# Optimization experiments

Measured on AMD Instinct MI355X. Metric: run time of the kernel, lower is better.

Reference implementation:

```python
import jax, jax.numpy as jnp
import numpy as np
from jax import lax

B, T, K = 1024, 512, 32


def setup_inputs() -> dict:
    key = jax.random.key(0)
    k1, k2, k3 = jax.random.split(key, 3)
    labels = jax.random.randint(k1, (B, T), 0, K, dtype=jnp.int32)
    y_pred = jax.random.normal(k2, (B, T, K), dtype=jnp.float32)
    # glorot-uniform-ish transition matrix
    limit = np.sqrt(6.0 / (K + K)).astype(np.float32)
    trans = jax.random.uniform(k3, (K, K), minval=-limit, maxval=limit, dtype=jnp.float32)
    mask = jnp.ones((B, T), dtype=jnp.float32)
    return {"labels": labels, "y_pred": y_pred, "trans": trans, "mask": mask}


def crf_loss(labels, y_pred, trans, mask):
    n_tags = trans.shape[0]
    y_true = jax.nn.one_hot(labels, n_tags, dtype=y_pred.dtype)  # [B,T,K]
    y_true = y_true * mask[:, :, None]  # sequence_masking with value 0

    # --- target path score ---
    point_score = jnp.einsum('bni,bni->b', y_true, y_pred)
    trans_score = jnp.einsum('bni,ij,bnj->b', y_true[:, :-1], trans, y_true[:, 1:])
    target = point_score + trans_score

    # --- log partition via forward algorithm (logsumexp scan) ---
    alpha0 = y_pred[:, 0]  # [B,K]

    def step(alpha, xs):
        emit, m = xs  # emit: [B,K], m: [B,1]
        new = jax.nn.logsumexp(alpha[:, :, None] + trans[None], axis=1) + emit
        alpha = m * new + (1.0 - m) * alpha
        return alpha, None

    xs = (jnp.swapaxes(y_pred[:, 1:], 0, 1),          # [T-1,B,K]
          jnp.swapaxes(mask[:, 1:, None], 0, 1))      # [T-1,B,1]
    alpha, _ = lax.scan(step, alpha0, xs)
    log_norm = jax.nn.logsumexp(alpha, axis=1)  # [B]
    return log_norm - target


def reference(labels, y_pred, trans, mask):
    return crf_loss(labels, y_pred, trans, mask)
```

## Files before the change

kernel.cpp:

```cpp
#include <hip/hip_runtime.h>


#define K32 32
#define Tt  512
#define NCH 4
#define CHL 128
#define NSEG 2

typedef float  float4v __attribute__((ext_vector_type(4)));
typedef short  short8v __attribute__((ext_vector_type(8)));

__device__ inline float bf2f_lo(unsigned d) { return __uint_as_float(d << 16); }
__device__ inline float bf2f_hi(unsigned d) { return __uint_as_float(d & 0xFFFF0000u); }

__device__ inline unsigned pack_trunc(float hi, float lo) {
    return __builtin_amdgcn_perm(__float_as_uint(hi), __float_as_uint(lo), 0x07060302u);
}
__device__ inline unsigned short f2bf_rne(float x) {
    unsigned u = __float_as_uint(x);
    return (unsigned short)((u + 0x7FFFu + ((u >> 16) & 1u)) >> 16);
}

union F8 { unsigned u[4]; short8v v; };

__global__ __launch_bounds__(256, 4) void crf_fused(
    const int*   __restrict__ labels,
    const float* __restrict__ y_pred,
    const float* __restrict__ trans,
    const float* __restrict__ mask,
    float*       __restrict__ out)
{
    __shared__ float expAll[4][2048];

    const int lane = threadIdx.x & 63;
    const int wv   = __builtin_amdgcn_readfirstlane(threadIdx.x >> 6);
    const int n    = lane & 15;
    const int q    = lane >> 4;
    const int seq  = blockIdx.x;
    const int c    = wv;

    float* eb = &expAll[wv][0];

    const float* yp  = y_pred + (size_t)seq * Tt * K32;
    const int*   lb  = labels + (size_t)seq * Tt;
    const float* mkp = mask   + (size_t)seq * Tt;
    const int tbase = c * CHL;

    float4 pre[8];
    {
        const float4* gs = (const float4*)(yp + (size_t)tbase * K32);
#pragma unroll
        for (int jj = 0; jj < 8; ++jj) pre[jj] = gs[jj * 64 + lane];
    }

    unsigned long long mb[NSEG];
    float sc = 0.0f;
#pragma unroll
    for (int s = 0; s < NSEG; ++s) {
        const int t = tbase + s * 64 + lane;
        const int lab0 = lb[t];
        const float mlane = mkp[t];
        float scl = yp[t * K32 + lab0] * mlane;
        if (t < Tt - 1) {
            scl += trans[lab0 * K32 + lb[t + 1]] * (mlane * mkp[t + 1]);
        }
        sc += scl;
        mb[s] = __ballot(mlane != 0.0f);
    }
    if (c == 0) mb[0] &= ~1ull;
#pragma unroll
    for (int s = 1; s < 64; s <<= 1) sc += __shfl_xor(sc, s, 64);

    F8 AE0, AE1;
#pragma unroll
    for (int h = 0; h < 4; ++h) {
        const int k0 = (h < 2) ? (q * 4 + 2 * h) : (16 + q * 4 + 2 * (h - 2));
        const int k1 = k0 + 1;
        AE0.u[h] = ((unsigned)f2bf_rne(__expf(trans[k0 * K32 + n]) * 0.03125f)) |
                   (((unsigned)f2bf_rne(__expf(trans[k1 * K32 + n]) * 0.03125f)) << 16);
        AE1.u[h] = ((unsigned)f2bf_rne(__expf(trans[k0 * K32 + 16 + n]) * 0.03125f)) |
                   (((unsigned)f2bf_rne(__expf(trans[k1 * K32 + 16 + n]) * 0.03125f)) << 16);
    }

    F8 B0, B1;
#pragma unroll
    for (int h = 0; h < 4; ++h) {
        const int r0 = (h < 2) ? (q * 4 + 2 * h) : (16 + q * 4 + 2 * (h - 2));
        const int r1 = r0 + 1;
        unsigned w0 = 0, w1 = 0;
        if (r0 == n)      w0 |= 0x3F80u;
        if (r1 == n)      w0 |= 0x3F800000u;
        if (r0 == 16 + n) w1 |= 0x3F80u;
        if (r1 == 16 + n) w1 |= 0x3F800000u;
        B0.u[h] = w0;
        B1.u[h] = w1;
    }

    float Slog    = 0.0f;
    int   applied = 0;

    const int svoff0 = q * 4;
    const int svoff1 = 16 + q * 4;

    auto body = [&](int i) {
        const float4v sv0 = *(const float4v*)&eb[i * 32 + svoff0];
        const float4v sv1 = *(const float4v*)&eb[i * 32 + svoff1];

        float4v c00 = {0.f, 0.f, 0.f, 0.f}, c01 = {0.f, 0.f, 0.f, 0.f};
        float4v c10 = {0.f, 0.f, 0.f, 0.f}, c11 = {0.f, 0.f, 0.f, 0.f};
        c00 = __builtin_amdgcn_mfma_f32_16x16x32_bf16(AE0.v, B0.v, c00, 0, 0, 0);
        c01 = __builtin_amdgcn_mfma_f32_16x16x32_bf16(AE0.v, B1.v, c01, 0, 0, 0);
        c10 = __builtin_amdgcn_mfma_f32_16x16x32_bf16(AE1.v, B0.v, c10, 0, 0, 0);
        c11 = __builtin_amdgcn_mfma_f32_16x16x32_bf16(AE1.v, B1.v, c11, 0, 0, 0);

        c00 *= sv0; c01 *= sv0; c10 *= sv1; c11 *= sv1;

        if ((applied & 7) == 7) {
            const float cn = __uint_as_float(
                __builtin_amdgcn_readfirstlane(__float_as_uint(c00[0])));
            const float rs = 1.0f / cn;
            c00 *= rs; c01 *= rs; c10 *= rs; c11 *= rs;
            Slog += __logf(cn);
        }
        ++applied;

        B0.u[0] = pack_trunc(c00[1], c00[0]);
        B0.u[1] = pack_trunc(c00[3], c00[2]);
        B0.u[2] = pack_trunc(c10[1], c10[0]);
        B0.u[3] = pack_trunc(c10[3], c10[2]);
        B1.u[0] = pack_trunc(c01[1], c01[0]);
        B1.u[1] = pack_trunc(c01[3], c01[2]);
        B1.u[2] = pack_trunc(c11[1], c11[0]);
        B1.u[3] = pack_trunc(c11[3], c11[2]);
    };

    for (int seg = 0; seg < NSEG; ++seg) {
#pragma unroll
        for (int jj = 0; jj < 8; ++jj) {
            float4v e;
            e[0] = __expf(pre[jj].x); e[1] = __expf(pre[jj].y);
            e[2] = __expf(pre[jj].z); e[3] = __expf(pre[jj].w);
            *(float4v*)&eb[(jj * 64 + lane) * 4] = e;
        }
        if (seg + 1 < NSEG) {
            const float4* gs = (const float4*)(yp + (size_t)(tbase + (seg + 1) * 64) * K32);
#pragma unroll
            for (int jj = 0; jj < 8; ++jj) pre[jj] = gs[jj * 64 + lane];
        }

        const unsigned long long mbits = mb[seg];
        if (mbits == ~0ull) {
#pragma unroll 8
            for (int i = 0; i < 64; ++i) body(i);
        } else {
#pragma unroll 4
            for (int i = 0; i < 64; ++i) {
                if ((mbits >> i) & 1ull) body(i);
            }
        }
    }

    {
        unsigned* Nd = (unsigned*)eb + 1024;
        *(uint2*)&Nd[n * 20 + q * 2]            = make_uint2(B0.u[0], B0.u[1]);
        *(uint2*)&Nd[n * 20 + 8 + q * 2]        = make_uint2(B0.u[2], B0.u[3]);
        *(uint2*)&Nd[(16 + n) * 20 + q * 2]     = make_uint2(B1.u[0], B1.u[1]);
        *(uint2*)&Nd[(16 + n) * 20 + 8 + q * 2] = make_uint2(B1.u[2], B1.u[3]);
    }
    {
        const unsigned short* Ncm = (const unsigned short*)((unsigned*)eb + 1024);
        unsigned* md = (unsigned*)eb;
        for (int idx = lane; idx < 512; idx += 64) {
            const int k = idx >> 4, d = idx & 15;
            const unsigned lo = Ncm[(2 * d) * 40 + k];
            const unsigned hi = Ncm[(2 * d + 1) * 40 + k];
            md[idx] = lo | (hi << 16);
        }
    }
    if (lane == 0) {
        eb[1984] = Slog + (float)applied * 3.46573590f;
        eb[1985] = sc;
    }

    __syncthreads();

    if (wv == 0) {
        const int h = lane >> 5;
        const int j = lane & 31;

        uint4 mA[NCH], mB[NCH];
#pragma unroll
        for (int cc = 0; cc < NCH; ++cc) {
            const unsigned* mt = (const unsigned*)&expAll[cc][0];
            mA[cc] = *(const uint4*)&mt[j * 16 + 8 * h];
            mB[cc] = *(const uint4*)&mt[j * 16 + 8 * h + 4];
        }

        const float a0 = yp[j];
        const float m0 = __shfl(a0, 0, 64);
        float p = __expf(a0 - m0);
        float S = m0;

        float scs = 0.0f;
#pragma unroll
        for (int cc = 0; cc < NCH; ++cc) {
            S   += expAll[cc][1984];
            scs += expAll[cc][1985];
        }

        const int cb = h << 4;
#pragma unroll
        for (int cc = 0; cc < NCH; ++cc) {
            const float cn = __shfl(p, 0, 64);
            const unsigned u0 = mA[cc].x, u1 = mA[cc].y, u2 = mA[cc].z, u3 = mA[cc].w;
            const unsigned u4 = mB[cc].x, u5 = mB[cc].y, u6 = mB[cc].z, u7 = mB[cc].w;
            float acc = 0.0f;
            acc = fmaf(__shfl(p, cb +  0, 64), bf2f_lo(u0), acc);
            acc = fmaf(__shfl(p, cb +  1, 64), bf2f_hi(u0), acc);
            acc = fmaf(__shfl(p, cb +  2, 64), bf2f_lo(u1), acc);
            acc = fmaf(__shfl(p, cb +  3, 64), bf2f_hi(u1), acc);
            acc = fmaf(__shfl(p, cb +  4, 64), bf2f_lo(u2), acc);
            acc = fmaf(__shfl(p, cb +  5, 64), bf2f_hi(u2), acc);
            acc = fmaf(__shfl(p, cb +  6, 64), bf2f_lo(u3), acc);
            acc = fmaf(__shfl(p, cb +  7, 64), bf2f_hi(u3), acc);
            acc = fmaf(__shfl(p, cb +  8, 64), bf2f_lo(u4), acc);
            acc = fmaf(__shfl(p, cb +  9, 64), bf2f_hi(u4), acc);
            acc = fmaf(__shfl(p, cb + 10, 64), bf2f_lo(u5), acc);
            acc = fmaf(__shfl(p, cb + 11, 64), bf2f_hi(u5), acc);
            acc = fmaf(__shfl(p, cb + 12, 64), bf2f_lo(u6), acc);
            acc = fmaf(__shfl(p, cb + 13, 64), bf2f_hi(u6), acc);
            acc = fmaf(__shfl(p, cb + 14, 64), bf2f_lo(u7), acc);
            acc = fmaf(__shfl(p, cb + 15, 64), bf2f_hi(u7), acc);
            acc += __shfl_xor(acc, 32, 64);
            p = acc * (1.0f / cn);
            S += __logf(cn);
        }

        float sp = p;
        sp += __shfl_xor(sp,  1, 64);
        sp += __shfl_xor(sp,  2, 64);
        sp += __shfl_xor(sp,  4, 64);
        sp += __shfl_xor(sp,  8, 64);
        sp += __shfl_xor(sp, 16, 64);

        if (lane == 0) {
            out[seq] = S + __logf(sp) - scs;
        }
    }
}

extern "C" void kernel_launch(void* const* d_in, const int* in_sizes, int n_in,
                              void* d_out, int out_size, void* d_ws, size_t ws_size,
                              hipStream_t stream) {
    const int*   labels = (const int*)  d_in[0];
    const float* y_pred = (const float*)d_in[1];
    const float* trans  = (const float*)d_in[2];
    const float* mask   = (const float*)d_in[3];
    float* out = (float*)d_out;

    crf_fused<<<1024, 256, 0, stream>>>(labels, y_pred, trans, mask, out);
}
```

Baseline: 141.5 us.

## Split each sequence into eight 64-step chunks across eight wavefronts

Each block now handles one sequence with 8 wavefronts, each running a 64-timestep chunk of the forward recurrence, where before 4 wavefronts each ran 128 steps. This halves the serial matrix-product chain per wave and uses 32-step staging of exp(emissions) without register prefetch. The cost is a longer final combine of 8 chunk matrices in wave 0, with the next matrix now loaded one step ahead inside that loop. It also raises block size and launch bounds, which adds register pressure.

After: 141.2 us. About the same (-0.2%).

```diff
diff --git a/kernel.cpp b/kernel.cpp
--- a/kernel.cpp
+++ b/kernel.cpp
@@ -3,9 +3,10 @@
 
 #define K32 32
 #define Tt  512
-#define NCH 4
-#define CHL 128
-#define NSEG 2
+#define NCH 8
+#define CHL 64
+#define NST 2
+#define STL 32
 
 typedef float  float4v __attribute__((ext_vector_type(4)));
 typedef short  short8v __attribute__((ext_vector_type(8)));
@@ -23,14 +24,14 @@
 
 union F8 { unsigned u[4]; short8v v; };
 
-__global__ __launch_bounds__(256, 4) void crf_fused(
+__global__ __launch_bounds__(512, 8) void crf_fused(
     const int*   __restrict__ labels,
     const float* __restrict__ y_pred,
     const float* __restrict__ trans,
     const float* __restrict__ mask,
     float*       __restrict__ out)
 {
-    __shared__ float expAll[4][2048];
+    __shared__ float expAll[8][1024];
 
     const int lane = threadIdx.x & 63;
     const int wv   = __builtin_amdgcn_readfirstlane(threadIdx.x >> 6);
@@ -46,30 +47,21 @@
     const float* mkp = mask   + (size_t)seq * Tt;
     const int tbase = c * CHL;
 
-    float4 pre[8];
+    float sc;
+    float mlane;
     {
-        const float4* gs = (const float4*)(yp + (size_t)tbase * K32);
-#pragma unroll
-        for (int jj = 0; jj < 8; ++jj) pre[jj] = gs[jj * 64 + lane];
-    }
-
-    unsigned long long mb[NSEG];
-    float sc = 0.0f;
-#pragma unroll
-    for (int s = 0; s < NSEG; ++s) {
-        const int t = tbase + s * 64 + lane;
+        const int t = tbase + lane;
         const int lab0 = lb[t];
-        const float mlane = mkp[t];
-        float scl = yp[t * K32 + lab0] * mlane;
+        mlane = mkp[t];
+        sc = yp[t * K32 + lab0] * mlane;
         if (t < Tt - 1) {
-            scl += trans[lab0 * K32 + lb[t + 1]] * (mlane * mkp[t + 1]);
-        }
-        sc += scl;
-        mb[s] = __ballot(mlane != 0.0f);
-    }
-    if (c == 0) mb[0] &= ~1ull;
-#pragma unroll
-    for (int s = 1; s < 64; s <<= 1) sc += __shfl_xor(sc, s, 64);
+            sc += trans[lab0 * K32 + lb[t + 1]] * (mlane * mkp[t + 1]);
+        }
+#pragma unroll
+        for (int s = 1; s < 64; s <<= 1) sc += __shfl_xor(sc, s, 64);
+    }
+    unsigned long long mbits = __ballot(mlane != 0.0f);
+    if (c == 0) mbits &= ~1ull;
 
     F8 AE0, AE1;
 #pragma unroll
@@ -134,52 +126,53 @@
         B1.u[3] = pack_trunc(c11[3], c11[2]);
     };
 
-    for (int seg = 0; seg < NSEG; ++seg) {
-#pragma unroll
-        for (int jj = 0; jj < 8; ++jj) {
+    for (int st = 0; st < NST; ++st) {
+        const float4* gs = (const float4*)(yp + (size_t)(tbase + st * STL) * K32);
+#pragma unroll
+        for (int jj = 0; jj < 4; ++jj) {
+            const float4 pv = gs[jj * 64 + lane];
             float4v e;
-            e[0] = __expf(pre[jj].x); e[1] = __expf(pre[jj].y);
-            e[2] = __expf(pre[jj].z); e[3] = __expf(pre[jj].w);
+            e[0] = __expf(pv.x); e[1] = __expf(pv.y);
+            e[2] = __expf(pv.z); e[3] = __expf(pv.w);
             *(float4v*)&eb[(jj * 64 + lane) * 4] = e;
         }
-        if (seg + 1 < NSEG) {
-            const float4* gs = (const float4*)(yp + (size_t)(tbase + (seg + 1) * 64) * K32);
-#pragma unroll
-            for (int jj = 0; jj < 8; ++jj) pre[jj] = gs[jj * 64 + lane];
-        }
-
-        const unsigned long long mbits = mb[seg];
-        if (mbits == ~0ull) {
+
+        const unsigned b32 = (unsigned)(mbits >> (st * 32));
+        if (b32 == 0xFFFFFFFFu) {
 #pragma unroll 8
-            for (int i = 0; i < 64; ++i) body(i);
+            for (int i = 0; i < STL; ++i) body(i);
         } else {
 #pragma unroll 4
-            for (int i = 0; i < 64; ++i) {
-                if ((mbits >> i) & 1ull) body(i);
+            for (int i = 0; i < STL; ++i) {
+                if ((b32 >> i) & 1u) body(i);
             }
         }
     }
 
     {
-        unsigned* Nd = (unsigned*)eb + 1024;
+        unsigned* Nd = (unsigned*)eb;
         *(uint2*)&Nd[n * 20 + q * 2]            = make_uint2(B0.u[0], B0.u[1]);
         *(uint2*)&Nd[n * 20 + 8 + q * 2]        = make_uint2(B0.u[2], B0.u[3]);
         *(uint2*)&Nd[(16 + n) * 20 + q * 2]     = make_uint2(B1.u[0], B1.u[1]);
         *(uint2*)&Nd[(16 + n) * 20 + 8 + q * 2] = make_uint2(B1.u[2], B1.u[3]);
     }
     {
-        const unsigned short* Ncm = (const unsigned short*)((unsigned*)eb + 1024);
+        const unsigned short* Ncm = (const unsigned short*)eb;
+        unsigned r[8];
+#pragma unroll
+        for (int ii = 0; ii < 8; ++ii) {
+            const int idx = ii * 64 + lane;
+            const int k = idx >> 4, d = idx & 15;
+            r[ii] = (unsigned)Ncm[(2 * d) * 40 + k] |
+                    ((unsigned)Ncm[(2 * d + 1) * 40 + k] << 16);
+        }
         unsigned* md = (unsigned*)eb;
-        for (int idx = lane; idx < 512; idx += 64) {
-            const int k = idx >> 4, d = idx & 15;
-            const unsigned lo = Ncm[(2 * d) * 40 + k];
-            const unsigned hi = Ncm[(2 * d + 1) * 40 + k];
-            md[idx] = lo | (hi << 16);
-        }
+#pragma unroll
+        for (int ii = 0; ii < 8; ++ii) md[ii * 64 + lane] = r[ii];
     }
     if (lane == 0) {
-        eb[1984] = Slog + (float)applied * 3.46573590f;
-        eb[1985] = sc;
+        eb[1016] = Slog + (float)applied * 3.46573590f;
+        eb[1017] = sc;
     }
 
     __syncthreads();
@@ -188,12 +181,11 @@
         const int h = lane >> 5;
         const int j = lane & 31;
 
-        uint4 mA[NCH], mB[NCH];
-#pragma unroll
-        for (int cc = 0; cc < NCH; ++cc) {
-            const unsigned* mt = (const unsigned*)&expAll[cc][0];
-            mA[cc] = *(const uint4*)&mt[j * 16 + 8 * h];
-            mB[cc] = *(const uint4*)&mt[j * 16 + 8 * h + 4];
+        uint4 cA, cB;
+        {
+            const unsigned* mt = (const unsigned*)&expAll[0][0];
+            cA = *(const uint4*)&mt[j * 16 + 8 * h];
+            cB = *(const uint4*)&mt[j * 16 + 8 * h + 4];
         }
 
         const float a0 = yp[j];
@@ -204,16 +196,22 @@
         float scs = 0.0f;
 #pragma unroll
         for (int cc = 0; cc < NCH; ++cc) {
-            S   += expAll[cc][1984];
-            scs += expAll[cc][1985];
+            S   += expAll[cc][1016];
+            scs += expAll[cc][1017];
         }
 
         const int cb = h << 4;
 #pragma unroll
         for (int cc = 0; cc < NCH; ++cc) {
+            uint4 nA = {0, 0, 0, 0}, nB = {0, 0, 0, 0};
+            if (cc + 1 < NCH) {
+                const unsigned* mt = (const unsigned*)&expAll[cc + 1][0];
+                nA = *(const uint4*)&mt[j * 16 + 8 * h];
+                nB = *(const uint4*)&mt[j * 16 + 8 * h + 4];
+            }
             const float cn = __shfl(p, 0, 64);
-            const unsigned u0 = mA[cc].x, u1 = mA[cc].y, u2 = mA[cc].z, u3 = mA[cc].w;
-            const unsigned u4 = mB[cc].x, u5 = mB[cc].y, u6 = mB[cc].z, u7 = mB[cc].w;
+            const unsigned u0 = cA.x, u1 = cA.y, u2 = cA.z, u3 = cA.w;
+            const unsigned u4 = cB.x, u5 = cB.y, u6 = cB.z, u7 = cB.w;
             float acc = 0.0f;
             acc = fmaf(__shfl(p, cb +  0, 64), bf2f_lo(u0), acc);
             acc = fmaf(__shfl(p, cb +  1, 64), bf2f_hi(u0), acc);
@@ -234,6 +232,7 @@
             acc += __shfl_xor(acc, 32, 64);
             p = acc * (1.0f / cn);
             S += __logf(cn);
+            cA = nA; cB = nB;
         }
 
         float sp = p;
@@ -258,5 +257,5 @@
     const float* mask   = (const float*)d_in[3];
     float* out = (float*)d_out;
 
-    crf_fused<<<1024, 256, 0, stream>>>(labels, y_pred, trans, mask, out);
-}
+    crf_fused<<<1024, 512, 0, stream>>>(labels, y_pred, trans, mask, out);
+}
```

## Batch 16 sequences per wave in serial MFMA scan, split score kernel

Applied to the files above, without the earlier changes.

Replaces the chunked per-sequence matrix-product scan with one wave per group of 16 sequences. The wave performs a serial matrix-vector forward recursion using MFMA, with double-buffered global loads and exponent-based renormalisation. The target path score moves into a separate kernel that writes to workspace. This removes the chunk-combine phase and the shared-memory staging, but it launches only 64 single-wave blocks and runs a 511-step serial dependency chain, which risks low occupancy and exposed memory latency.

Result: slower. 171.8 us (+21.4%).

```diff
diff --git a/kernel.cpp b/kernel.cpp
--- a/kernel.cpp
+++ b/kernel.cpp
@@ -3,9 +3,7 @@
 
 #define K32 32
 #define Tt  512
-#define NCH 4
-#define CHL 128
-#define NSEG 2
+#define SB  16
 
 typedef float  float4v __attribute__((ext_vector_type(4)));
 typedef short  short8v __attribute__((ext_vector_type(8)));
@@ -23,229 +21,199 @@
 
 union F8 { unsigned u[4]; short8v v; };
 
-__global__ __launch_bounds__(256, 4) void crf_fused(
+__global__ __launch_bounds__(64) void crf_score(
     const int*   __restrict__ labels,
     const float* __restrict__ y_pred,
     const float* __restrict__ trans,
     const float* __restrict__ mask,
+    float*       __restrict__ wsScore)
+{
+    const int s    = blockIdx.x;
+    const int lane = threadIdx.x;
+    const int*   lb  = labels + (size_t)s * Tt;
+    const float* mkp = mask   + (size_t)s * Tt;
+    const float* yp  = y_pred + (size_t)s * Tt * K32;
+
+    float sc = 0.0f;
+#pragma unroll
+    for (int j = 0; j < 8; ++j) {
+        const int t   = j * 64 + lane;
+        const int lab = lb[t];
+        const float m = mkp[t];
+        sc += yp[t * K32 + lab] * m;
+        if (t < Tt - 1) sc += trans[lab * K32 + lb[t + 1]] * (m * mkp[t + 1]);
+    }
+#pragma unroll
+    for (int sft = 1; sft < 64; sft <<= 1) sc += __shfl_xor(sc, sft, 64);
+    if (lane == 0) wsScore[s] = sc;
+}
+
+__global__ __launch_bounds__(64) void crf_scan(
+    const float* __restrict__ y_pred,
+    const float* __restrict__ trans,
+    const float* __restrict__ mask,
+    const float* __restrict__ wsScore,
     float*       __restrict__ out)
 {
-    __shared__ float expAll[4][2048];
-
-    const int lane = threadIdx.x & 63;
-    const int wv   = __builtin_amdgcn_readfirstlane(threadIdx.x >> 6);
+    const int lane = threadIdx.x;
     const int n    = lane & 15;
-    const int q    = lane >> 4;
-    const int seq  = blockIdx.x;
-    const int c    = wv;
-
-    float* eb = &expAll[wv][0];
-
-    const float* yp  = y_pred + (size_t)seq * Tt * K32;
-    const int*   lb  = labels + (size_t)seq * Tt;
-    const float* mkp = mask   + (size_t)seq * Tt;
-    const int tbase = c * CHL;
-
-    float4 pre[8];
+    const int g    = lane >> 4;
+    const int sb   = blockIdx.x * SB;
+
+    const float* yp_n = y_pred + (size_t)(sb + n) * Tt * K32;
+    const float* mk_n = mask   + (size_t)(sb + n) * Tt;
+
+    F8 Alo, Ahi;
+#pragma unroll
+    for (int h = 0; h < 4; ++h) {
+        const int k0 = (h < 2) ? (g * 4 + 2 * h) : (16 + g * 4 + 2 * (h - 2));
+        const int k1 = k0 + 1;
+        Alo.u[h] = ((unsigned)f2bf_rne(__expf(trans[k0 * K32 + n]) * 0.03125f)) |
+                   (((unsigned)f2bf_rne(__expf(trans[k1 * K32 + n]) * 0.03125f)) << 16);
+        Ahi.u[h] = ((unsigned)f2bf_rne(__expf(trans[k0 * K32 + 16 + n]) * 0.03125f)) |
+                   (((unsigned)f2bf_rne(__expf(trans[k1 * K32 + 16 + n]) * 0.03125f)) << 16);
+    }
+
+    bool allones;
     {
-        const float4* gs = (const float4*)(yp + (size_t)tbase * K32);
-#pragma unroll
-        for (int jj = 0; jj < 8; ++jj) pre[jj] = gs[jj * 64 + lane];
-    }
-
-    unsigned long long mb[NSEG];
-    float sc = 0.0f;
-#pragma unroll
-    for (int s = 0; s < NSEG; ++s) {
-        const int t = tbase + s * 64 + lane;
-        const int lab0 = lb[t];
-        const float mlane = mkp[t];
-        float scl = yp[t * K32 + lab0] * mlane;
-        if (t < Tt - 1) {
-            scl += trans[lab0 * K32 + lb[t + 1]] * (mlane * mkp[t + 1]);
-        }
-        sc += scl;
-        mb[s] = __ballot(mlane != 0.0f);
-    }
-    if (c == 0) mb[0] &= ~1ull;
-#pragma unroll
-    for (int s = 1; s < 64; s <<= 1) sc += __shfl_xor(sc, s, 64);
-
-    F8 AE0, AE1;
-#pragma unroll
-    for (int h = 0; h < 4; ++h) {
-        const int k0 = (h < 2) ? (q * 4 + 2 * h) : (16 + q * 4 + 2 * (h - 2));
-        const int k1 = k0 + 1;
-        AE0.u[h] = ((unsigned)f2bf_rne(__expf(trans[k0 * K32 + n]) * 0.03125f)) |
-                   (((unsigned)f2bf_rne(__expf(trans[k1 * K32 + n]) * 0.03125f)) << 16);
-        AE1.u[h] = ((unsigned)f2bf_rne(__expf(trans[k0 * K32 + 16 + n]) * 0.03125f)) |
-                   (((unsigned)f2bf_rne(__expf(trans[k1 * K32 + 16 + n]) * 0.03125f)) << 16);
-    }
-
-    F8 B0, B1;
-#pragma unroll
-    for (int h = 0; h < 4; ++h) {
-        const int r0 = (h < 2) ? (q * 4 + 2 * h) : (16 + q * 4 + 2 * (h - 2));
-        const int r1 = r0 + 1;
-        unsigned w0 = 0, w1 = 0;
-        if (r0 == n)      w0 |= 0x3F80u;
-        if (r1 == n)      w0 |= 0x3F800000u;
-        if (r0 == 16 + n) w1 |= 0x3F80u;
-        if (r1 == 16 + n) w1 |= 0x3F800000u;
-        B0.u[h] = w0;
-        B1.u[h] = w1;
-    }
-
-    float Slog    = 0.0f;
-    int   applied = 0;
-
-    const int svoff0 = q * 4;
-    const int svoff1 = 16 + q * 4;
-
-    auto body = [&](int i) {
-        const float4v sv0 = *(const float4v*)&eb[i * 32 + svoff0];
-        const float4v sv1 = *(const float4v*)&eb[i * 32 + svoff1];
-
-        float4v c00 = {0.f, 0.f, 0.f, 0.f}, c01 = {0.f, 0.f, 0.f, 0.f};
-        float4v c10 = {0.f, 0.f, 0.f, 0.f}, c11 = {0.f, 0.f, 0.f, 0.f};
-        c00 = __builtin_amdgcn_mfma_f32_16x16x32_bf16(AE0.v, B0.v, c00, 0, 0, 0);
-        c01 = __builtin_amdgcn_mfma_f32_16x16x32_bf16(AE0.v, B1.v, c01, 0, 0, 0);
-        c10 = __builtin_amdgcn_mfma_f32_16x16x32_bf16(AE1.v, B0.v, c10, 0, 0, 0);
-        c11 = __builtin_amdgcn_mfma_f32_16x16x32_bf16(AE1.v, B1.v, c11, 0, 0, 0);
-
-        c00 *= sv0; c01 *= sv0; c10 *= sv1; c11 *= sv1;
-
-        if ((applied & 7) == 7) {
-            const float cn = __uint_as_float(
-                __builtin_amdgcn_readfirstlane(__float_as_uint(c00[0])));
-            const float rs = 1.0f / cn;
-            c00 *= rs; c01 *= rs; c10 *= rs; c11 *= rs;
-            Slog += __logf(cn);
-        }
-        ++applied;
-
-        B0.u[0] = pack_trunc(c00[1], c00[0]);
-        B0.u[1] = pack_trunc(c00[3], c00[2]);
-        B0.u[2] = pack_trunc(c10[1], c10[0]);
-        B0.u[3] = pack_trunc(c10[3], c10[2]);
-        B1.u[0] = pack_trunc(c01[1], c01[0]);
-        B1.u[1] = pack_trunc(c01[3], c01[2]);
-        B1.u[2] = pack_trunc(c11[1], c11[0]);
-        B1.u[3] = pack_trunc(c11[3], c11[2]);
+        float mn = 1.0f;
+        const float4* m4 = (const float4*)(mk_n + g * 128);
+#pragma unroll
+        for (int j = 0; j < 32; ++j) {
+            const float4 v = m4[j];
+            mn = fminf(mn, fminf(fminf(v.x, v.y), fminf(v.z, v.w)));
+        }
+        allones = (__ballot(mn == 1.0f) == ~0ull);
+    }
+
+    const float4v zf = {0.f, 0.f, 0.f, 0.f};
+    F8 V;
+    int eSum    = 0;
+    int applied = 0;
+
+    float4 bufA[16], bufB[16];
+
+    auto LOADG = [&](float4 (&buf)[16], int grp) {
+#pragma unroll
+        for (int i = 0; i < 8; ++i) {
+            const int t = grp * 8 + i;
+            buf[2 * i]     = *(const float4*)(yp_n + t * K32 + 4 * g);
+            buf[2 * i + 1] = *(const float4*)(yp_n + t * K32 + 16 + 4 * g);
+        }
     };
 
-    for (int seg = 0; seg < NSEG; ++seg) {
-#pragma unroll
-        for (int jj = 0; jj < 8; ++jj) {
-            float4v e;
-            e[0] = __expf(pre[jj].x); e[1] = __expf(pre[jj].y);
-            e[2] = __expf(pre[jj].z); e[3] = __expf(pre[jj].w);
-            *(float4v*)&eb[(jj * 64 + lane) * 4] = e;
-        }
-        if (seg + 1 < NSEG) {
-            const float4* gs = (const float4*)(yp + (size_t)(tbase + (seg + 1) * 64) * K32);
-#pragma unroll
-            for (int jj = 0; jj < 8; ++jj) pre[jj] = gs[jj * 64 + lane];
-        }
-
-        const unsigned long long mbits = mb[seg];
-        if (mbits == ~0ull) {
-#pragma unroll 8
-            for (int i = 0; i < 64; ++i) body(i);
-        } else {
-#pragma unroll 4
-            for (int i = 0; i < 64; ++i) {
-                if ((mbits >> i) & 1ull) body(i);
-            }
-        }
-    }
-
+    LOADG(bufA, 0);
     {
-        unsigned* Nd = (unsigned*)eb + 1024;
-        *(uint2*)&Nd[n * 20 + q * 2]            = make_uint2(B0.u[0], B0.u[1]);
-        *(uint2*)&Nd[n * 20 + 8 + q * 2]        = make_uint2(B0.u[2], B0.u[3]);
-        *(uint2*)&Nd[(16 + n) * 20 + q * 2]     = make_uint2(B1.u[0], B1.u[1]);
-        *(uint2*)&Nd[(16 + n) * 20 + 8 + q * 2] = make_uint2(B1.u[2], B1.u[3]);
-    }
-    {
-        const unsigned short* Ncm = (const unsigned short*)((unsigned*)eb + 1024);
-        unsigned* md = (unsigned*)eb;
-        for (int idx = lane; idx < 512; idx += 64) {
-            const int k = idx >> 4, d = idx & 15;
-            const unsigned lo = Ncm[(2 * d) * 40 + k];
-            const unsigned hi = Ncm[(2 * d + 1) * 40 + k];
-            md[idx] = lo | (hi << 16);
-        }
-    }
-    if (lane == 0) {
-        eb[1984] = Slog + (float)applied * 3.46573590f;
-        eb[1985] = sc;
-    }
-
-    __syncthreads();
-
-    if (wv == 0) {
-        const int h = lane >> 5;
-        const int j = lane & 31;
-
-        uint4 mA[NCH], mB[NCH];
-#pragma unroll
-        for (int cc = 0; cc < NCH; ++cc) {
-            const unsigned* mt = (const unsigned*)&expAll[cc][0];
-            mA[cc] = *(const uint4*)&mt[j * 16 + 8 * h];
-            mB[cc] = *(const uint4*)&mt[j * 16 + 8 * h + 4];
-        }
-
-        const float a0 = yp[j];
-        const float m0 = __shfl(a0, 0, 64);
-        float p = __expf(a0 - m0);
-        float S = m0;
-
-        float scs = 0.0f;
-#pragma unroll
-        for (int cc = 0; cc < NCH; ++cc) {
-            S   += expAll[cc][1984];
-            scs += expAll[cc][1985];
-        }
-
-        const int cb = h << 4;
-#pragma unroll
-        for (int cc = 0; cc < NCH; ++cc) {
-            const float cn = __shfl(p, 0, 64);
-            const unsigned u0 = mA[cc].x, u1 = mA[cc].y, u2 = mA[cc].z, u3 = mA[cc].w;
-            const unsigned u4 = mB[cc].x, u5 = mB[cc].y, u6 = mB[cc].z, u7 = mB[cc].w;
-            float acc = 0.0f;
-            acc = fmaf(__shfl(p, cb +  0, 64), bf2f_lo(u0), acc);
-            acc = fmaf(__shfl(p, cb +  1, 64), bf2f_hi(u0), acc);
-            acc = fmaf(__shfl(p, cb +  2, 64), bf2f_lo(u1), acc);
-            acc = fmaf(__shfl(p, cb +  3, 64), bf2f_hi(u1), acc);
-            acc = fmaf(__shfl(p, cb +  4, 64), bf2f_lo(u2), acc);
-            acc = fmaf(__shfl(p, cb +  5, 64), bf2f_hi(u2), acc);
-            acc = fmaf(__shfl(p, cb +  6, 64), bf2f_lo(u3), acc);
-            acc = fmaf(__shfl(p, cb +  7, 64), bf2f_hi(u3), acc);
-            acc = fmaf(__shfl(p, cb +  8, 64), bf2f_lo(u4), acc);
-            acc = fmaf(__shfl(p, cb +  9, 64), bf2f_hi(u4), acc);
-            acc = fmaf(__shfl(p, cb + 10, 64), bf2f_lo(u5), acc);
-            acc = fmaf(__shfl(p, cb + 11, 64), bf2f_hi(u5), acc);
-            acc = fmaf(__shfl(p, cb + 12, 64), bf2f_lo(u6), acc);
-            acc = fmaf(__shfl(p, cb + 13, 64), bf2f_hi(u6), acc);
-            acc = fmaf(__shfl(p, cb + 14, 64), bf2f_lo(u7), acc);
-            acc = fmaf(__shfl(p, cb + 15, 64), bf2f_hi(u7), acc);
-            acc += __shfl_xor(acc, 32, 64);
-            p = acc * (1.0f / cn);
-            S += __logf(cn);
-        }
-
-        float sp = p;
-        sp += __shfl_xor(sp,  1, 64);
-        sp += __shfl_xor(sp,  2, 64);
-        sp += __shfl_xor(sp,  4, 64);
-        sp += __shfl_xor(sp,  8, 64);
-        sp += __shfl_xor(sp, 16, 64);
-
-        if (lane == 0) {
-            out[seq] = S + __logf(sp) - scs;
-        }
+        const float4 lo = bufA[0], hi = bufA[1];
+        V.u[0] = pack_trunc(__expf(lo.y), __expf(lo.x));
+        V.u[1] = pack_trunc(__expf(lo.w), __expf(lo.z));
+        V.u[2] = pack_trunc(__expf(hi.y), __expf(hi.x));
+        V.u[3] = pack_trunc(__expf(hi.w), __expf(hi.z));
+    }
+    LOADG(bufB, 1);
+
+    auto stepf = [&](const float4 lo, const float4 hi, bool ren) {
+        float4v cl = __builtin_amdgcn_mfma_f32_16x16x32_bf16(Alo.v, V.v, zf, 0, 0, 0);
+        float4v ch = __builtin_amdgcn_mfma_f32_16x16x32_bf16(Ahi.v, V.v, zf, 0, 0, 0);
+        const float4v d0 = {__expf(lo.x), __expf(lo.y), __expf(lo.z), __expf(lo.w)};
+        const float4v d1 = {__expf(hi.x), __expf(hi.y), __expf(hi.z), __expf(hi.w)};
+        cl *= d0; ch *= d1;
+        if (ren) {
+            const float rb = __shfl(cl[0], n, 64);
+            const int e = (int)((__float_as_uint(rb) >> 23) & 255u) - 127;
+            const float rs = __uint_as_float((unsigned)(127 - e) << 23);
+            cl *= rs; ch *= rs;
+            eSum += e;
+        }
+        V.u[0] = pack_trunc(cl[1], cl[0]);
+        V.u[1] = pack_trunc(cl[3], cl[2]);
+        V.u[2] = pack_trunc(ch[1], ch[0]);
+        V.u[3] = pack_trunc(ch[3], ch[2]);
+    };
+
+    auto stepm = [&](const float4 lo, const float4 hi, int t, bool ren) {
+        const float m  = mk_n[t];
+        const bool vm  = (m != 0.0f);
+        float4v cl = __builtin_amdgcn_mfma_f32_16x16x32_bf16(Alo.v, V.v, zf, 0, 0, 0);
+        float4v ch = __builtin_amdgcn_mfma_f32_16x16x32_bf16(Ahi.v, V.v, zf, 0, 0, 0);
+        const float4v d0 = {__expf(lo.x), __expf(lo.y), __expf(lo.z), __expf(lo.w)};
+        const float4v d1 = {__expf(hi.x), __expf(hi.y), __expf(hi.z), __expf(hi.w)};
+        cl *= d0; ch *= d1;
+        if (ren) {
+            const float rb = __shfl(cl[0], n, 64);
+            int e = (int)((__float_as_uint(rb) >> 23) & 255u) - 127;
+            e = vm ? e : 0;
+            const float rs = __uint_as_float((unsigned)(127 - e) << 23);
+            cl *= rs; ch *= rs;
+            eSum += e;
+        }
+        const unsigned v0 = pack_trunc(cl[1], cl[0]);
+        const unsigned v1 = pack_trunc(cl[3], cl[2]);
+        const unsigned v2 = pack_trunc(ch[1], ch[0]);
+        const unsigned v3 = pack_trunc(ch[3], ch[2]);
+        V.u[0] = vm ? v0 : V.u[0];
+        V.u[1] = vm ? v1 : V.u[1];
+        V.u[2] = vm ? v2 : V.u[2];
+        V.u[3] = vm ? v3 : V.u[3];
+        applied += vm ? 1 : 0;
+    };
+
+    if (allones) {
+        applied = Tt - 1;
+        for (int bb = 0; bb < 32; ++bb) {
+            if (bb > 0) stepf(bufA[0], bufA[1], false);
+            stepf(bufA[2],  bufA[3],  false);
+            stepf(bufA[4],  bufA[5],  false);
+            stepf(bufA[6],  bufA[7],  false);
+            stepf(bufA[8],  bufA[9],  false);
+            stepf(bufA[10], bufA[11], false);
+            stepf(bufA[12], bufA[13], false);
+            stepf(bufA[14], bufA[15], true);
+            if (bb < 31) LOADG(bufA, 2 * bb + 2);
+            stepf(bufB[0],  bufB[1],  false);
+            stepf(bufB[2],  bufB[3],  false);
+            stepf(bufB[4],  bufB[5],  false);
+            stepf(bufB[6],  bufB[7],  false);
+            stepf(bufB[8],  bufB[9],  false);
+            stepf(bufB[10], bufB[11], false);
+            stepf(bufB[12], bufB[13], false);
+            stepf(bufB[14], bufB[15], true);
+            if (bb < 31) LOADG(bufB, 2 * bb + 3);
+        }
+    } else {
+        for (int bb = 0; bb < 32; ++bb) {
+            const int tA = bb * 16, tB = tA + 8;
+            if (bb > 0) stepm(bufA[0], bufA[1], tA + 0, false);
+            stepm(bufA[2],  bufA[3],  tA + 1, false);
+            stepm(bufA[4],  bufA[5],  tA + 2, false);
+            stepm(bufA[6],  bufA[7],  tA + 3, false);
+            stepm(bufA[8],  bufA[9],  tA + 4, false);
+            stepm(bufA[10], bufA[11], tA + 5, false);
+            stepm(bufA[12], bufA[13], tA + 6, false);
+            stepm(bufA[14], bufA[15], tA + 7, true);
+            if (bb < 31) LOADG(bufA, 2 * bb + 2);
+            stepm(bufB[0],  bufB[1],  tB + 0, false);
+            stepm(bufB[2],  bufB[3],  tB + 1, false);
+            stepm(bufB[4],  bufB[5],  tB + 2, false);
+            stepm(bufB[6],  bufB[7],  tB + 3, false);
+            stepm(bufB[8],  bufB[9],  tB + 4, false);
+            stepm(bufB[10], bufB[11], tB + 5, false);
+            stepm(bufB[12], bufB[13], tB + 6, false);
+            stepm(bufB[14], bufB[15], tB + 7, true);
+            if (bb < 31) LOADG(bufB, 2 * bb + 3);
+        }
+    }
+
+    float ssum = bf2f_lo(V.u[0]) + bf2f_hi(V.u[0]) +
+                 bf2f_lo(V.u[1]) + bf2f_hi(V.u[1]) +
+                 bf2f_lo(V.u[2]) + bf2f_hi(V.u[2]) +
+                 bf2f_lo(V.u[3]) + bf2f_hi(V.u[3]);
+    ssum += __shfl_xor(ssum, 16, 64);
+    ssum += __shfl_xor(ssum, 32, 64);
+
+    if (lane < 16) {
+        out[sb + n] = __logf(ssum) + (float)eSum * 0.693147180559945f +
+                      (float)applied * 3.46573590f - wsScore[sb + n];
     }
 }
 
@@ -257,6 +225,8 @@
     const float* trans  = (const float*)d_in[2];
     const float* mask   = (const float*)d_in[3];
     float* out = (float*)d_out;
-
-    crf_fused<<<1024, 256, 0, stream>>>(labels, y_pred, trans, mask, out);
-}
+    float* wsScore = (float*)d_ws;
+
+    crf_score<<<1024, 64, 0, stream>>>(labels, y_pred, trans, mask, wsScore);
+    crf_scan<<<64, 64, 0, stream>>>(y_pred, trans, mask, wsScore, out);
+}
```
